# Kernel optimization log

Measured on AMD Instinct MI355X. Metric: run time of the kernel, lower is better.

The kernel has to match this reference:

```python
import jax, jax.numpy as jnp
import numpy as np

WARP_WEIGHT = 2.5   # level 2
MD = 3              # max displacement -> 7x7 = 49 correlation channels
NEG_SLOPE = 0.1


def setup_inputs() -> dict:
    key = jax.random.key(0)
    ks = jax.random.split(key, 9)
    B, C, H, W = 8, 128, 128, 128
    features1 = jax.random.normal(ks[0], (B, C, H, W), jnp.float32)
    features2 = jax.random.normal(ks[1], (B, C, H, W), jnp.float32)
    flow = jax.random.normal(ks[2], (B, 2, H // 2, W // 2), jnp.float32)

    def conv_w(k, o, i, kh, kw):
        bound = 1.0 / np.sqrt(i * kh * kw)
        return jax.random.uniform(k, (o, i, kh, kw), jnp.float32, -bound, bound)

    def conv_b(k, o, i, kh, kw):
        bound = 1.0 / np.sqrt(i * kh * kw)
        return jax.random.uniform(k, (o,), jnp.float32, -bound, bound)

    return {
        "features1": features1,
        "features2": features2,
        "flow": flow,
        "w1": conv_w(ks[3], 64, 49, 3, 3), "b1": conv_b(ks[4], 64, 49, 3, 3),
        "w2": conv_w(ks[5], 32, 64, 3, 3), "b2": conv_b(ks[6], 32, 64, 3, 3),
        "w3": conv_w(ks[7], 2, 32, 5, 5),  "b3": conv_b(ks[8], 2, 32, 5, 5),
    }


def _resize_bilinear(x, h, w):
    # matches torch interpolate(mode='bilinear', align_corners=False)
    B, C = x.shape[:2]
    return jax.image.resize(x, (B, C, h, w), method="bilinear")


def _warp(img, fl):
    # backward warp: sample img at (x + fl_x, y + fl_y), bilinear, zeros outside
    B, C, H, W = img.shape
    yy, xx = jnp.meshgrid(jnp.arange(H, dtype=jnp.float32),
                          jnp.arange(W, dtype=jnp.float32), indexing="ij")
    x = xx[None] + fl[:, 0]   # [B,H,W]
    y = yy[None] + fl[:, 1]
    x0f, y0f = jnp.floor(x), jnp.floor(y)
    wx, wy = x - x0f, y - y0f
    x0, y0 = x0f.astype(jnp.int32), y0f.astype(jnp.int32)

    def gather(yi, xi):
        valid = (yi >= 0) & (yi < H) & (xi >= 0) & (xi < W)
        yc = jnp.clip(yi, 0, H - 1)
        xc = jnp.clip(xi, 0, W - 1)
        v = jax.vmap(lambda im, a, b: im[:, a, b])(img, yc, xc)  # [B,C,H,W]
        return v * valid[:, None].astype(img.dtype)

    return (gather(y0, x0) * ((1 - wx) * (1 - wy))[:, None]
            + gather(y0, x0 + 1) * (wx * (1 - wy))[:, None]
            + gather(y0 + 1, x0) * ((1 - wx) * wy)[:, None]
            + gather(y0 + 1, x0 + 1) * (wx * wy)[:, None])


def _correlation(f1, f2):
    # windowed cost volume: out[b, dy*7+dx] = mean_c f1[b,c,y,x]*f2[b,c,y+dy-3,x+dx-3]
    B, C, H, W = f1.shape
    f2p = jnp.pad(f2, ((0, 0), (0, 0), (MD, MD), (MD, MD)))
    outs = [jnp.mean(f1 * f2p[:, :, dy:dy + H, dx:dx + W], axis=1)
            for dy in range(2 * MD + 1) for dx in range(2 * MD + 1)]
    return jnp.stack(outs, axis=1)  # [B,49,H,W]


def _conv(x, w, b, pad):
    y = jax.lax.conv_general_dilated(
        x, w, window_strides=(1, 1), padding=[(pad, pad), (pad, pad)],
        dimension_numbers=("NCHW", "OIHW", "NCHW"))
    return y + b[None, :, None, None]


def _lrelu(x):
    return jnp.where(x >= 0, x, NEG_SLOPE * x)


def reference(features1, features2, flow, w1, b1, w2, b2, w3, b3):
    H, W = features1.shape[-2:]
    flow_up = _resize_bilinear(flow, H, W)                 # [B,2,H,W]
    f2w = _warp(features2, flow_up * WARP_WEIGHT)
    corr = _correlation(features1, f2w)                    # [B,49,H,W]
    h = _lrelu(_conv(corr, w1, b1, 1))
    h = _lrelu(_conv(h, w2, b2, 1))
    h = _conv(h, w3, b3, 2)                                # [B,2,H,W]
    return flow_up + h
```

## Files before the change

### kernel.cpp

```cpp
#include <hip/hip_runtime.h>
#include <hip/hip_bf16.h>

#define BB 8
#define CC 128
#define HH 128
#define WW 128
#define HW (HH*WW)
#define MD 3
#define ND 49
#define WARP_WEIGHT 2.5f
#define NEG 0.1f

typedef __attribute__((ext_vector_type(8))) short bf16x8;
typedef __attribute__((ext_vector_type(4))) float f32x4;

__device__ inline ushort f2bf(float f) {
    __hip_bfloat16 h = __float2bfloat16(f);
    return *reinterpret_cast<ushort*>(&h);
}
__device__ inline float bf2f(short s) {
    return __uint_as_float(((uint)(ushort)s) << 16);
}

#define G8_IDX(b, y, g) ((((size_t)((b) * HH + (y)) * 16) + (g)) * (WW * 8))

__global__ void k_flow_up(const float* __restrict__ flow, float* __restrict__ flow_up) {
    const int x = threadIdx.x;
    const int y = blockIdx.x;
    const int c = blockIdx.y;
    const int b = blockIdx.z;
    const int Hs = 64, Ws = 64;
    float sy = (y + 0.5f) * 0.5f - 0.5f;
    float sx = (x + 0.5f) * 0.5f - 0.5f;
    float y0f = floorf(sy), x0f = floorf(sx);
    int y0 = (int)y0f, x0 = (int)x0f;
    float wy = sy - y0f, wx = sx - x0f;
    int y0c = min(max(y0, 0), Hs - 1), y1c = min(max(y0 + 1, 0), Hs - 1);
    int x0c = min(max(x0, 0), Ws - 1), x1c = min(max(x0 + 1, 0), Ws - 1);
    const float* src = flow + ((size_t)(b * 2 + c)) * Hs * Ws;
    float v00 = src[y0c * Ws + x0c], v01 = src[y0c * Ws + x1c];
    float v10 = src[y1c * Ws + x0c], v11 = src[y1c * Ws + x1c];
    float v = v00 * (1.f - wx) * (1.f - wy) + v01 * wx * (1.f - wy)
            + v10 * (1.f - wx) * wy + v11 * wx * wy;
    flow_up[((size_t)(b * 2 + c) * HH + y) * WW + x] = v;
}

__global__ __launch_bounds__(256) void k_prep_cl(const float* __restrict__ src,
                                                 ushort* __restrict__ dstcl) {
    __shared__ ushort lds[128][68];
    const int y = blockIdx.x & 127;
    const int b = (blockIdx.x >> 7) & 7;
    const int chunk = blockIdx.x >> 10;
    {
        const int x = threadIdx.x & 127;
        const int cg = threadIdx.x >> 7;
        const int c0 = chunk * 64 + cg * 32;
        const float* s = src + ((size_t)b * CC + c0) * HW + y * WW + x;
#pragma unroll
        for (int j4 = 0; j4 < 8; j4++) {
            ushort t[4];
#pragma unroll
            for (int u = 0; u < 4; u++) t[u] = f2bf(s[(size_t)(j4 * 4 + u) * HW]);
            *reinterpret_cast<uint2*>(&lds[x][cg * 32 + j4 * 4]) =
                *reinterpret_cast<const uint2*>(t);
        }
    }
    __syncthreads();
    {
        const int xw = threadIdx.x >> 1;
        const int h = threadIdx.x & 1;
        ushort* d = dstcl + (((size_t)(b * HH + y)) * WW + xw) * CC + chunk * 64 + h * 32;
#pragma unroll
        for (int i = 0; i < 8; i++)
            *reinterpret_cast<uint2*>(d + i * 4) =
                *reinterpret_cast<const uint2*>(&lds[xw][h * 32 + i * 4]);
    }
}

__global__ __launch_bounds__(256) void k_warp2(const ushort* __restrict__ f2cl,
                                               const float* __restrict__ flow_up,
                                               ushort* __restrict__ f2wg8) {
    const int bid = blockIdx.x;
    const int k = bid & 7;
    const int t = bid >> 3;
    const int xs = t & 7;
    const int y  = k * 16 + ((t >> 3) & 15);
    const int b  = t >> 7;
    const int p  = threadIdx.x >> 4;
    const int g  = threadIdx.x & 15;
    const int x  = xs * 16 + p;

    const float fx = flow_up[((size_t)(b * 2 + 0) * HH + y) * WW + x] * WARP_WEIGHT;
    const float fy = flow_up[((size_t)(b * 2 + 1) * HH + y) * WW + x] * WARP_WEIGHT;
    const float sx = (float)x + fx;
    const float sy = (float)y + fy;
    float x0f = floorf(sx), y0f = floorf(sy);
    int x0 = (int)x0f, y0 = (int)y0f;
    float wx = sx - x0f, wy = sy - y0f;
    int x0c = min(max(x0, 0), WW - 1), x1c = min(max(x0 + 1, 0), WW - 1);
    int y0c = min(max(y0, 0), HH - 1), y1c = min(max(y0 + 1, 0), HH - 1);
    bool vx0 = (x0 >= 0) & (x0 < WW);
    bool vx1 = (x0 + 1 >= 0) & (x0 + 1 < WW);
    bool vy0 = (y0 >= 0) & (y0 < HH);
    bool vy1 = (y0 + 1 >= 0) & (y0 + 1 < HH);
    float w00 = (vx0 && vy0) ? (1.f - wx) * (1.f - wy) : 0.f;
    float w01 = (vx1 && vy0) ? wx * (1.f - wy) : 0.f;
    float w10 = (vx0 && vy1) ? (1.f - wx) * wy : 0.f;
    float w11 = (vx1 && vy1) ? wx * wy : 0.f;

    const ushort* base = f2cl + (size_t)b * HW * CC + (size_t)g * 8;
    bf16x8 t00 = *reinterpret_cast<const bf16x8*>(base + ((size_t)y0c * WW + x0c) * CC);
    bf16x8 t01 = *reinterpret_cast<const bf16x8*>(base + ((size_t)y0c * WW + x1c) * CC);
    bf16x8 t10 = *reinterpret_cast<const bf16x8*>(base + ((size_t)y1c * WW + x0c) * CC);
    bf16x8 t11 = *reinterpret_cast<const bf16x8*>(base + ((size_t)y1c * WW + x1c) * CC);

    ushort o[8];
#pragma unroll
    for (int j = 0; j < 8; j++) {
        float v = w00 * bf2f(t00[j]) + w01 * bf2f(t01[j])
                + w10 * bf2f(t10[j]) + w11 * bf2f(t11[j]);
        o[j] = f2bf(v);
    }
    *reinterpret_cast<uint4*>(f2wg8 + G8_IDX(b, y, g) + x * 8) =
        *reinterpret_cast<const uint4*>(o);
}

__global__ __launch_bounds__(512) void k_corr_mfma(const float* __restrict__ f1,
                                                   const ushort* __restrict__ f2g8,
                                                   ushort* __restrict__ Ct) {
    __shared__ __align__(16) ushort sbuf[16 * 128 * 8];
    __shared__ ushort cstage[128][68];
    const int b  = blockIdx.x & 7;
    const int y  = blockIdx.x >> 3;
    const int w  = threadIdx.x >> 6;
    const int l  = threadIdx.x & 63;
    const int lx = l & 15;
    const int lk = l >> 4;
    const int xa0 = w * 16;

    bf16x8 afr[4];
#pragma unroll
    for (int kk = 0; kk < 4; kk++) {
        const float* src = f1 + ((size_t)(b * CC + kk * 32 + lk * 8)) * HW
                         + y * WW + xa0 + lx;
        float tv[8];
#pragma unroll
        for (int j = 0; j < 8; j++) tv[j] = src[(size_t)j * HW];
        ushort tmp[8];
#pragma unroll
        for (int j = 0; j < 8; j++) tmp[j] = f2bf(tv[j]);
        afr[kk] = *reinterpret_cast<const bf16x8*>(tmp);
    }

    const int xb0 = xa0 - 3 + lx;
    const int xb1 = xa0 + 13 + lx;
    const int xc0 = min(max(xb0, 0), WW - 1);
    const int xc1 = min(max(xb1, 0), WW - 1);
    const bool xm0 = (unsigned)xb0 < (unsigned)WW;
    const bool xm1 = (unsigned)xb1 < (unsigned)WW;
    const bf16x8 zf = {};
    const float scale = 1.f / (float)CC;

    for (int dy = 0; dy < 7; dy++) {
        const int yy = y + dy - MD;
        const bool yv = (unsigned)yy < (unsigned)HH;
        if (yv) {
            const ushort* src = f2g8 + G8_IDX(b, yy, 0) + threadIdx.x * 8;
            ushort* dst = sbuf + threadIdx.x * 8;
#pragma unroll
            for (int i = 0; i < 4; i++)
                *reinterpret_cast<uint4*>(dst + i * 4096) =
                    *reinterpret_cast<const uint4*>(src + i * 4096);
        }
        __syncthreads();

        f32x4 acc0 = (f32x4)(0.f), acc1 = (f32x4)(0.f);
        if (yv) {
#pragma unroll
            for (int kk = 0; kk < 4; kk++) {
                const ushort* grp = sbuf + (kk * 4 + lk) * (WW * 8);
                bf16x8 b0 = *reinterpret_cast<const bf16x8*>(grp + xc0 * 8);
                bf16x8 b1 = *reinterpret_cast<const bf16x8*>(grp + xc1 * 8);
                b0 = xm0 ? b0 : zf;
                b1 = xm1 ? b1 : zf;
                acc0 = __builtin_amdgcn_mfma_f32_16x16x32_bf16(afr[kk], b0, acc0, 0, 0, 0);
                acc1 = __builtin_amdgcn_mfma_f32_16x16x32_bf16(afr[kk], b1, acc1, 0, 0, 0);
            }
        }
#pragma unroll
        for (int r = 0; r < 4; r++) {
            const int i = lk * 4 + r;
            const int d0 = lx - i;
            if (d0 >= 0 && d0 <= 6)
                cstage[xa0 + i][dy * 7 + d0] = f2bf(acc0[r] * scale);
            const int d1 = lx - i + 16;
            if (d1 >= 0 && d1 <= 6)
                cstage[xa0 + i][dy * 7 + d1] = f2bf(acc1[r] * scale);
        }
        __syncthreads();
    }

    {
        const int row = xa0 + (l >> 2);
        const int part = l & 3;
        ushort* dst = Ct + (((size_t)(b * HH + y)) * WW + row) * 64 + part * 16;
        if (part < 3) {
            uint2 t0 = *reinterpret_cast<const uint2*>(&cstage[row][part * 16 + 0]);
            uint2 t1 = *reinterpret_cast<const uint2*>(&cstage[row][part * 16 + 4]);
            uint2 t2 = *reinterpret_cast<const uint2*>(&cstage[row][part * 16 + 8]);
            uint2 t3 = *reinterpret_cast<const uint2*>(&cstage[row][part * 16 + 12]);
            uint4 v0; v0.x = t0.x; v0.y = t0.y; v0.z = t1.x; v0.w = t1.y;
            uint4 v1; v1.x = t2.x; v1.y = t2.y; v1.z = t3.x; v1.w = t3.y;
            *reinterpret_cast<uint4*>(dst) = v0;
            *reinterpret_cast<uint4*>(dst + 8) = v1;
        } else {
            uint4 v0; v0.x = (uint)cstage[row][48]; v0.y = 0u; v0.z = 0u; v0.w = 0u;
            uint4 v1; v1.x = 0u; v1.y = 0u; v1.z = 0u; v1.w = 0u;
            *reinterpret_cast<uint4*>(dst) = v0;
            *reinterpret_cast<uint4*>(dst + 8) = v1;
        }
    }
}

template<int IC, int ICP, int OC, int OCP, int KK>
__global__ void k_prep_w2(const float* __restrict__ w, ushort* __restrict__ Wt) {
    constexpr int NCH = ICP / 32;
    int e = blockIdx.x * 256 + threadIdx.x;
    const int total = KK * KK * NCH * 4 * OCP * 8;
    if (e >= total) return;
    int j  = e & 7;
    int oc = (e >> 3) % OCP;
    int lk = (e / (8 * OCP)) & 3;
    int t  = e / (8 * OCP * 4);
    int ch = t % NCH;
    int tap = t / NCH;
    int kh = tap / KK, kw = tap % KK;
    int c = ch * 32 + lk * 8 + j;
    float v = 0.f;
    if (oc < OC && c < IC) v = w[((oc * IC + c) * KK + kh) * KK + kw];
    Wt[e] = f2bf(v);
}

template<int ICP, int OCP, int MT, int NT, int OCOUT, int KK, int PAD, bool RELU, bool LAST>
__global__ __launch_bounds__(512, 4) void k_conv_lds(
    const ushort* __restrict__ In, const ushort* __restrict__ Wt,
    const float* __restrict__ bias, ushort* __restrict__ Out,
    const float* __restrict__ flow_up, float* __restrict__ fout)
{
    constexpr int NCH = ICP / 32;
    constexpr int NTAP = KK * KK * NCH;
    constexpr int ROWB = ICP * 2;
    constexpr int ROWBYTES = WW * ROWB;
    constexpr int NROWS = KK + 1;
    constexpr int SLAB = NROWS * ROWBYTES;
    constexpr int LOG2ROWB = (ICP == 64) ? 7 : 6;
    constexpr int SWZM = (ICP == 64) ? 7 : 3;
    constexpr int ITER = SLAB / (512 * 16);

    __shared__ __align__(16) char slds[SLAB];

    const int y0 = blockIdx.x * 2;
    const int b = blockIdx.y;
    const char* inb = (const char*)(In + (size_t)b * HH * WW * ICP);

#pragma unroll
    for (int it = 0; it < ITER; it++) {
        int L = it * 512 * 16 + threadIdx.x * 16;
        int r = L / ROWBYTES;
        int Lr = L % ROWBYTES;
        int grow = min(max(y0 - PAD + r, 0), HH - 1);
        uint4 v = *reinterpret_cast<const uint4*>(inb + (size_t)grow * ROWBYTES + Lr);
        int dst = r * ROWBYTES + (Lr ^ (((Lr >> LOG2ROWB) & SWZM) << 4));
        *reinterpret_cast<uint4*>(&slds[dst]) = v;
    }
    __syncthreads();

    const int w = threadIdx.x >> 6;
    const int l = threadIdx.x & 63;
    const int lx = l & 15;
    const int lk = l >> 4;
    const int wr = w >> 2;
    const int wq = w & 3;
    const int y = y0 + wr;
    const int n0 = wq * (16 * NT);

    f32x4 acc[MT][NT];
#pragma unroll
    for (int m = 0; m < MT; m++)
#pragma unroll
        for (int nt = 0; nt < NT; nt++) acc[m][nt] = (f32x4)(0.f);

    bf16x8 abuf[2][MT];
    auto load_a = [&](int t, int buf) {
#pragma unroll
        for (int m = 0; m < MT; m++)
            abuf[buf][m] = *reinterpret_cast<const bf16x8*>(
                Wt + ((size_t)(t * 4 + lk) * OCP + m * 16 + lx) * 8);
    };

    load_a(0, 0);
#pragma unroll
    for (int t = 0; t < NTAP; t++) {
        if (t + 1 < NTAP) load_a(t + 1, (t + 1) & 1);
        const int kh = t / (KK * NCH);
        const int kw = (t / NCH) % KK;
        const int ch = t % NCH;
        const int slab_r = wr + kh;
        const int yy = y + kh - PAD;
        const bool yv = (unsigned)yy < (unsigned)HH;
        bf16x8 bfr[NT];
#pragma unroll
        for (int nt = 0; nt < NT; nt++) {
            int xx = n0 + nt * 16 + lx + kw - PAD;
            int xc = min(max(xx, 0), WW - 1);
            int off = slab_r * ROWBYTES
                    + ((xc * ROWB + (ch * 4 + lk) * 16) ^ ((xc & SWZM) << 4));
            bf16x8 v = *reinterpret_cast<const bf16x8*>(&slds[off]);
            bool valid = yv && ((unsigned)xx < (unsigned)WW);
            bfr[nt] = valid ? v : (bf16x8){};
        }
#pragma unroll
        for (int nt = 0; nt < NT; nt++)
#pragma unroll
            for (int m = 0; m < MT; m++)
                acc[m][nt] = __builtin_amdgcn_mfma_f32_16x16x32_bf16(
                    abuf[t & 1][m], bfr[nt], acc[m][nt], 0, 0, 0);
    }

    if (!LAST) {
#pragma unroll
        for (int m = 0; m < MT; m++) {
            const int oc0 = m * 16 + lk * 4;
            float4 bs = *reinterpret_cast<const float4*>(bias + oc0);
#pragma unroll
            for (int nt = 0; nt < NT; nt++) {
                int x = n0 + nt * 16 + lx;
                float v0 = acc[m][nt][0] + bs.x;
                float v1 = acc[m][nt][1] + bs.y;
                float v2 = acc[m][nt][2] + bs.z;
                float v3 = acc[m][nt][3] + bs.w;
                if (RELU) {
                    v0 = (v0 >= 0.f) ? v0 : NEG * v0;
                    v1 = (v1 >= 0.f) ? v1 : NEG * v1;
                    v2 = (v2 >= 0.f) ? v2 : NEG * v2;
                    v3 = (v3 >= 0.f) ? v3 : NEG * v3;
                }
                ushort4 o;
                o.x = f2bf(v0); o.y = f2bf(v1); o.z = f2bf(v2); o.w = f2bf(v3);
                *reinterpret_cast<ushort4*>(Out + (((size_t)(b * HH + y)) * WW + x) * OCOUT + oc0) = o;
            }
        }
    } else {
        if (lk == 0) {
#pragma unroll
            for (int nt = 0; nt < NT; nt++) {
                int x = n0 + nt * 16 + lx;
#pragma unroll
                for (int r = 0; r < 2; r++) {
                    size_t o = (((size_t)(b * 2 + r)) * HH + y) * WW + x;
                    fout[o] = acc[0][nt][r] + bias[r] + flow_up[o];
                }
            }
        }
    }
}

extern "C" void kernel_launch(void* const* d_in, const int* in_sizes, int n_in,
                              void* d_out, int out_size, void* d_ws, size_t ws_size,
                              hipStream_t stream) {
    const float* f1   = (const float*)d_in[0];
    const float* f2   = (const float*)d_in[1];
    const float* flow = (const float*)d_in[2];
    const float* w1   = (const float*)d_in[3];
    const float* b1   = (const float*)d_in[4];
    const float* w2   = (const float*)d_in[5];
    const float* b2   = (const float*)d_in[6];
    const float* w3   = (const float*)d_in[7];
    const float* b3   = (const float*)d_in[8];
    float* out = (float*)d_out;

    char* ws = (char*)d_ws;
    const size_t SZ_FLOWUP = (size_t)BB * 2 * HW * 4;
    const size_t SZ_CT     = (size_t)BB * HW * 64 * 2;
    const size_t SZ_WT1    = (size_t)9 * 2 * 4 * 64 * 8 * 2;
    const size_t SZ_WT2    = (size_t)9 * 2 * 4 * 32 * 8 * 2;
    const size_t SZ_WT3    = (size_t)25 * 1 * 4 * 16 * 8 * 2;
    const size_t SZ_BUF    = (size_t)BB * HW * CC * 2;

    float*  flow_up = (float*)ws;                         ws += SZ_FLOWUP;
    ushort* Ct      = (ushort*)ws;                        ws += SZ_CT;
    ushort* Wt1     = (ushort*)ws;                        ws += SZ_WT1;
    ushort* Wt2     = (ushort*)ws;                        ws += SZ_WT2;
    ushort* Wt3     = (ushort*)ws;                        ws += SZ_WT3;
    ushort* f2wg8   = (ushort*)ws;                        ws += SZ_BUF;
    ushort* bufA    = (ushort*)ws;
    ushort* f2cl    = bufA;
    ushort* h1      = bufA;
    ushort* h2      = (ushort*)((char*)bufA + (size_t)BB * HW * 64 * 2);

    k_prep_w2<49, 64, 64, 64, 3><<<dim3((9 * 2 * 4 * 64 * 8 + 255) / 256), dim3(256), 0, stream>>>(w1, Wt1);
    k_prep_w2<64, 64, 32, 32, 3><<<dim3((9 * 2 * 4 * 32 * 8 + 255) / 256), dim3(256), 0, stream>>>(w2, Wt2);
    k_prep_w2<32, 32, 2, 16, 5><<<dim3((25 * 1 * 4 * 16 * 8 + 255) / 256), dim3(256), 0, stream>>>(w3, Wt3);

    k_flow_up<<<dim3(HH, 2, BB), dim3(WW), 0, stream>>>(flow, flow_up);
    k_prep_cl<<<dim3(2048), dim3(256), 0, stream>>>(f2, f2cl);
    k_warp2  <<<dim3(8192), dim3(256), 0, stream>>>(f2cl, flow_up, f2wg8);
    k_corr_mfma<<<dim3(1024), dim3(512), 0, stream>>>(f1, f2wg8, Ct);

    k_conv_lds<64, 64, 4, 2, 64, 3, 1, true,  false>
        <<<dim3(HH / 2, BB), dim3(512), 0, stream>>>(Ct, Wt1, b1, h1, nullptr, nullptr);
    k_conv_lds<64, 32, 2, 2, 32, 3, 1, true,  false>
        <<<dim3(HH / 2, BB), dim3(512), 0, stream>>>(h1, Wt2, b2, h2, nullptr, nullptr);
    k_conv_lds<32, 16, 1, 2, 2,  5, 2, false, true >
        <<<dim3(HH / 2, BB), dim3(512), 0, stream>>>(h2, Wt3, b3, nullptr, flow_up, out);
}
```

Measured before the change: 121.0 us.

## Double-buffer correlation row loads in shared memory with register prefetch

The correlation kernel now splits each displaced f2 row into two half-channel stages and keeps them in a two-slot shared buffer. The next stage's global loads are issued into registers before the current stage's MFMAs and committed to shared memory afterwards, so load latency overlaps compute. The cost is more loop iterations and barriers (14 instead of 7), a smaller per-stage working set, and more register pressure from the prefetch registers.

```diff
diff --git a/kernel.cpp b/kernel.cpp
--- a/kernel.cpp
+++ b/kernel.cpp
@@ -128,7 +128,7 @@
 __global__ __launch_bounds__(512) void k_corr_mfma(const float* __restrict__ f1,
                                                    const ushort* __restrict__ f2g8,
                                                    ushort* __restrict__ Ct) {
-    __shared__ __align__(16) ushort sbuf[16 * 128 * 8];
+    __shared__ __align__(16) ushort sbuf[2][8 * 128 * 8];
     __shared__ ushort cstage[128][68];
     const int b  = blockIdx.x & 7;
     const int y  = blockIdx.x >> 3;
@@ -161,24 +161,40 @@
     const bf16x8 zf = {};
     const float scale = 1.f / (float)CC;
 
-    for (int dy = 0; dy < 7; dy++) {
-        const int yy = y + dy - MD;
-        const bool yv = (unsigned)yy < (unsigned)HH;
+    uint4 r0, r1;
+    auto issue = [&](int s) {
+        const int ry = y + (s >> 1) - MD;
+        const ushort* src = f2g8 + G8_IDX(b, ry, (s & 1) * 8) + threadIdx.x * 8;
+        r0 = *reinterpret_cast<const uint4*>(src);
+        r1 = *reinterpret_cast<const uint4*>(src + 4096);
+    };
+    auto commit = [&](int s) {
+        ushort* dst = &sbuf[s & 1][threadIdx.x * 8];
+        *reinterpret_cast<uint4*>(dst) = r0;
+        *reinterpret_cast<uint4*>(dst + 4096) = r1;
+    };
+    auto valid_s = [&](int s) {
+        const int ry = y + (s >> 1) - MD;
+        return (unsigned)ry < (unsigned)HH;
+    };
+
+    if (valid_s(0)) { issue(0); commit(0); }
+    __syncthreads();
+
+    f32x4 acc0 = (f32x4)(0.f), acc1 = (f32x4)(0.f);
+#pragma unroll
+    for (int s = 0; s < 14; s++) {
+        const int dy = s >> 1;
+        const int h = s & 1;
+        const bool yv = valid_s(s);
+        const bool nv = (s + 1 < 14) && valid_s(s + 1);
+        if (nv) issue(s + 1);
+        if (h == 0) { acc0 = (f32x4)(0.f); acc1 = (f32x4)(0.f); }
         if (yv) {
-            const ushort* src = f2g8 + G8_IDX(b, yy, 0) + threadIdx.x * 8;
-            ushort* dst = sbuf + threadIdx.x * 8;
-#pragma unroll
-            for (int i = 0; i < 4; i++)
-                *reinterpret_cast<uint4*>(dst + i * 4096) =
-                    *reinterpret_cast<const uint4*>(src + i * 4096);
-        }
-        __syncthreads();
-
-        f32x4 acc0 = (f32x4)(0.f), acc1 = (f32x4)(0.f);
-        if (yv) {
-#pragma unroll
-            for (int kk = 0; kk < 4; kk++) {
-                const ushort* grp = sbuf + (kk * 4 + lk) * (WW * 8);
+#pragma unroll
+            for (int kx = 0; kx < 2; kx++) {
+                const int kk = 2 * h + kx;
+                const ushort* grp = &sbuf[s & 1][(kx * 4 + lk) * (WW * 8)];
                 bf16x8 b0 = *reinterpret_cast<const bf16x8*>(grp + xc0 * 8);
                 bf16x8 b1 = *reinterpret_cast<const bf16x8*>(grp + xc1 * 8);
                 b0 = xm0 ? b0 : zf;
@@ -187,16 +203,19 @@
                 acc1 = __builtin_amdgcn_mfma_f32_16x16x32_bf16(afr[kk], b1, acc1, 0, 0, 0);
             }
         }
-#pragma unroll
-        for (int r = 0; r < 4; r++) {
-            const int i = lk * 4 + r;
-            const int d0 = lx - i;
-            if (d0 >= 0 && d0 <= 6)
-                cstage[xa0 + i][dy * 7 + d0] = f2bf(acc0[r] * scale);
-            const int d1 = lx - i + 16;
-            if (d1 >= 0 && d1 <= 6)
-                cstage[xa0 + i][dy * 7 + d1] = f2bf(acc1[r] * scale);
-        }
+        if (h == 1) {
+#pragma unroll
+            for (int r = 0; r < 4; r++) {
+                const int i = lk * 4 + r;
+                const int d0 = lx - i;
+                if (d0 >= 0 && d0 <= 6)
+                    cstage[xa0 + i][dy * 7 + d0] = f2bf(acc0[r] * scale);
+                const int d1 = lx - i + 16;
+                if (d1 >= 0 && d1 <= 6)
+                    cstage[xa0 + i][dy * 7 + d1] = f2bf(acc1[r] * scale);
+            }
+        }
+        if (nv) commit(s + 1);
         __syncthreads();
     }
 
```

New measurement: 122.5 us. Within noise of the previous version (+1.2%).

## Compute two output rows per correlation block to reuse staged f2 rows

Applied to the files above, without the earlier changes.

The correlation kernel now handles two adjacent output rows per block. Each wave covers 32 pixels of one row, and the block stages 8 f2 rows into LDS instead of 7 rows per single output row. This roughly halves the global and LDS traffic for the warped features and the number of block launches. In exchange it doubles the per-wave A-fragment registers, doubles the staging buffer, and leaves half the waves idle on the edge iterations of the shared row loop.

```diff
diff --git a/kernel.cpp b/kernel.cpp
--- a/kernel.cpp
+++ b/kernel.cpp
@@ -129,40 +129,52 @@
                                                    const ushort* __restrict__ f2g8,
                                                    ushort* __restrict__ Ct) {
     __shared__ __align__(16) ushort sbuf[16 * 128 * 8];
-    __shared__ ushort cstage[128][68];
+    __shared__ ushort cstage[2][128][68];
     const int b  = blockIdx.x & 7;
-    const int y  = blockIdx.x >> 3;
+    const int yq = blockIdx.x >> 3;
+    const int y0 = yq * 2;
     const int w  = threadIdx.x >> 6;
     const int l  = threadIdx.x & 63;
     const int lx = l & 15;
     const int lk = l >> 4;
-    const int xa0 = w * 16;
-
-    bf16x8 afr[4];
-#pragma unroll
-    for (int kk = 0; kk < 4; kk++) {
-        const float* src = f1 + ((size_t)(b * CC + kk * 32 + lk * 8)) * HW
-                         + y * WW + xa0 + lx;
-        float tv[8];
-#pragma unroll
-        for (int j = 0; j < 8; j++) tv[j] = src[(size_t)j * HW];
-        ushort tmp[8];
-#pragma unroll
-        for (int j = 0; j < 8; j++) tmp[j] = f2bf(tv[j]);
-        afr[kk] = *reinterpret_cast<const bf16x8*>(tmp);
-    }
-
-    const int xb0 = xa0 - 3 + lx;
-    const int xb1 = xa0 + 13 + lx;
-    const int xc0 = min(max(xb0, 0), WW - 1);
-    const int xc1 = min(max(xb1, 0), WW - 1);
-    const bool xm0 = (unsigned)xb0 < (unsigned)WW;
-    const bool xm1 = (unsigned)xb1 < (unsigned)WW;
+    const int r  = w >> 2;
+    const int q  = w & 3;
+    const int y  = y0 + r;
+
+    bf16x8 afr[2][4];
+#pragma unroll
+    for (int st = 0; st < 2; st++) {
+#pragma unroll
+        for (int kk = 0; kk < 4; kk++) {
+            const float* src = f1 + ((size_t)(b * CC + kk * 32 + lk * 8)) * HW
+                             + y * WW + q * 32 + st * 16 + lx;
+            float tv[8];
+#pragma unroll
+            for (int j = 0; j < 8; j++) tv[j] = src[(size_t)j * HW];
+            ushort tmp[8];
+#pragma unroll
+            for (int j = 0; j < 8; j++) tmp[j] = f2bf(tv[j]);
+            afr[st][kk] = *reinterpret_cast<const bf16x8*>(tmp);
+        }
+    }
+
+    int xc0[2], xc1[2];
+    bool xm0[2], xm1[2];
+#pragma unroll
+    for (int st = 0; st < 2; st++) {
+        const int base = q * 32 + st * 16;
+        const int b0 = base - 3 + lx;
+        const int b1 = base + 13 + lx;
+        xc0[st] = min(max(b0, 0), WW - 1);
+        xc1[st] = min(max(b1, 0), WW - 1);
+        xm0[st] = (unsigned)b0 < (unsigned)WW;
+        xm1[st] = (unsigned)b1 < (unsigned)WW;
+    }
     const bf16x8 zf = {};
     const float scale = 1.f / (float)CC;
 
-    for (int dy = 0; dy < 7; dy++) {
-        const int yy = y + dy - MD;
+    for (int s = 0; s < 8; s++) {
+        const int yy = y0 - 3 + s;
         const bool yv = (unsigned)yy < (unsigned)HH;
         if (yv) {
             const ushort* src = f2g8 + G8_IDX(b, yy, 0) + threadIdx.x * 8;
@@ -174,50 +186,74 @@
         }
         __syncthreads();
 
-        f32x4 acc0 = (f32x4)(0.f), acc1 = (f32x4)(0.f);
-        if (yv) {
-#pragma unroll
-            for (int kk = 0; kk < 4; kk++) {
-                const ushort* grp = sbuf + (kk * 4 + lk) * (WW * 8);
-                bf16x8 b0 = *reinterpret_cast<const bf16x8*>(grp + xc0 * 8);
-                bf16x8 b1 = *reinterpret_cast<const bf16x8*>(grp + xc1 * 8);
-                b0 = xm0 ? b0 : zf;
-                b1 = xm1 ? b1 : zf;
-                acc0 = __builtin_amdgcn_mfma_f32_16x16x32_bf16(afr[kk], b0, acc0, 0, 0, 0);
-                acc1 = __builtin_amdgcn_mfma_f32_16x16x32_bf16(afr[kk], b1, acc1, 0, 0, 0);
+        const int dy = s - r;
+        if (dy >= 0 && dy <= 6) {
+#pragma unroll
+            for (int st = 0; st < 2; st++) {
+                f32x4 acc0 = (f32x4)(0.f), acc1 = (f32x4)(0.f);
+                if (yv) {
+#pragma unroll
+                    for (int kk = 0; kk < 4; kk++) {
+                        const ushort* grp = sbuf + (kk * 4 + lk) * (WW * 8);
+                        bf16x8 b0 = *reinterpret_cast<const bf16x8*>(grp + xc0[st] * 8);
+                        bf16x8 b1 = *reinterpret_cast<const bf16x8*>(grp + xc1[st] * 8);
+                        b0 = xm0[st] ? b0 : zf;
+                        b1 = xm1[st] ? b1 : zf;
+                        acc0 = __builtin_amdgcn_mfma_f32_16x16x32_bf16(afr[st][kk], b0, acc0, 0, 0, 0);
+                        acc1 = __builtin_amdgcn_mfma_f32_16x16x32_bf16(afr[st][kk], b1, acc1, 0, 0, 0);
+                    }
+                }
+#pragma unroll
+                for (int rr = 0; rr < 4; rr++) {
+                    const int i = lk * 4 + rr;
+                    const int px = q * 32 + st * 16 + i;
+                    const int d0 = lx - i;
+                    if (d0 >= 0 && d0 <= 6)
+                        cstage[r][px][dy * 7 + d0] = f2bf(acc0[rr] * scale);
+                    const int d1 = lx - i + 16;
+                    if (d1 >= 0 && d1 <= 6)
+                        cstage[r][px][dy * 7 + d1] = f2bf(acc1[rr] * scale);
+                }
             }
         }
-#pragma unroll
-        for (int r = 0; r < 4; r++) {
-            const int i = lk * 4 + r;
-            const int d0 = lx - i;
-            if (d0 >= 0 && d0 <= 6)
-                cstage[xa0 + i][dy * 7 + d0] = f2bf(acc0[r] * scale);
-            const int d1 = lx - i + 16;
-            if (d1 >= 0 && d1 <= 6)
-                cstage[xa0 + i][dy * 7 + d1] = f2bf(acc1[r] * scale);
-        }
         __syncthreads();
     }
 
     {
-        const int row = xa0 + (l >> 2);
-        const int part = l & 3;
-        ushort* dst = Ct + (((size_t)(b * HH + y)) * WW + row) * 64 + part * 16;
-        if (part < 3) {
-            uint2 t0 = *reinterpret_cast<const uint2*>(&cstage[row][part * 16 + 0]);
-            uint2 t1 = *reinterpret_cast<const uint2*>(&cstage[row][part * 16 + 4]);
-            uint2 t2 = *reinterpret_cast<const uint2*>(&cstage[row][part * 16 + 8]);
-            uint2 t3 = *reinterpret_cast<const uint2*>(&cstage[row][part * 16 + 12]);
+        const int pxl = l >> 1;
+        const int px = q * 32 + pxl;
+        const int half = l & 1;
+        ushort* dst = Ct + (((size_t)(b * HH + y)) * WW + px) * 64 + half * 32;
+        if (half == 0) {
+            uint2 t0 = *reinterpret_cast<const uint2*>(&cstage[r][px][0]);
+            uint2 t1 = *reinterpret_cast<const uint2*>(&cstage[r][px][4]);
+            uint2 t2 = *reinterpret_cast<const uint2*>(&cstage[r][px][8]);
+            uint2 t3 = *reinterpret_cast<const uint2*>(&cstage[r][px][12]);
+            uint2 t4 = *reinterpret_cast<const uint2*>(&cstage[r][px][16]);
+            uint2 t5 = *reinterpret_cast<const uint2*>(&cstage[r][px][20]);
+            uint2 t6 = *reinterpret_cast<const uint2*>(&cstage[r][px][24]);
+            uint2 t7 = *reinterpret_cast<const uint2*>(&cstage[r][px][28]);
             uint4 v0; v0.x = t0.x; v0.y = t0.y; v0.z = t1.x; v0.w = t1.y;
             uint4 v1; v1.x = t2.x; v1.y = t2.y; v1.z = t3.x; v1.w = t3.y;
-            *reinterpret_cast<uint4*>(dst) = v0;
-            *reinterpret_cast<uint4*>(dst + 8) = v1;
+            uint4 v2; v2.x = t4.x; v2.y = t4.y; v2.z = t5.x; v2.w = t5.y;
+            uint4 v3; v3.x = t6.x; v3.y = t6.y; v3.z = t7.x; v3.w = t7.y;
+            *reinterpret_cast<uint4*>(dst + 0)  = v0;
+            *reinterpret_cast<uint4*>(dst + 8)  = v1;
+            *reinterpret_cast<uint4*>(dst + 16) = v2;
+            *reinterpret_cast<uint4*>(dst + 24) = v3;
         } else {
-            uint4 v0; v0.x = (uint)cstage[row][48]; v0.y = 0u; v0.z = 0u; v0.w = 0u;
-            uint4 v1; v1.x = 0u; v1.y = 0u; v1.z = 0u; v1.w = 0u;
-            *reinterpret_cast<uint4*>(dst) = v0;
-            *reinterpret_cast<uint4*>(dst + 8) = v1;
+            uint2 t0 = *reinterpret_cast<const uint2*>(&cstage[r][px][32]);
+            uint2 t1 = *reinterpret_cast<const uint2*>(&cstage[r][px][36]);
+            uint2 t2 = *reinterpret_cast<const uint2*>(&cstage[r][px][40]);
+            uint2 t3 = *reinterpret_cast<const uint2*>(&cstage[r][px][44]);
+            uint4 v0; v0.x = t0.x; v0.y = t0.y; v0.z = t1.x; v0.w = t1.y;
+            uint4 v1; v1.x = t2.x; v1.y = t2.y; v1.z = t3.x; v1.w = t3.y;
+            uint4 v2; v2.x = (uint)cstage[r][px][48]; v2.y = 0u; v2.z = 0u; v2.w = 0u;
+            uint4 v3; v3.x = 0u; v3.y = 0u; v3.z = 0u; v3.w = 0u;
+            *reinterpret_cast<uint4*>(dst + 0)  = v0;
+            *reinterpret_cast<uint4*>(dst + 8)  = v1;
+            *reinterpret_cast<uint4*>(dst + 16) = v2;
+            *reinterpret_cast<uint4*>(dst + 24) = v3;
         }
     }
 }
@@ -405,7 +441,7 @@
     k_flow_up<<<dim3(HH, 2, BB), dim3(WW), 0, stream>>>(flow, flow_up);
     k_prep_cl<<<dim3(2048), dim3(256), 0, stream>>>(f2, f2cl);
     k_warp2  <<<dim3(8192), dim3(256), 0, stream>>>(f2cl, flow_up, f2wg8);
-    k_corr_mfma<<<dim3(1024), dim3(512), 0, stream>>>(f1, f2wg8, Ct);
+    k_corr_mfma<<<dim3(512), dim3(512), 0, stream>>>(f1, f2wg8, Ct);
 
     k_conv_lds<64, 64, 4, 2, 64, 3, 1, true,  false>
         <<<dim3(HH / 2, BB), dim3(512), 0, stream>>>(Ct, Wt1, b1, h1, nullptr, nullptr);
```

Measured after the change: 127.7 us. +5.5%, slower.
